# Kernel tuning notes

Measured on AMD Instinct MI355X. Metric: run time of the kernel, lower is better.

Reference implementation:

```python
import jax, jax.numpy as jnp
import numpy as np

D_MODEL, D_K, D_V, H = 512, 64, 64, 8
B, NQ, NK = 16, 784, 784
HW = 28  # sqrt(NQ)


def setup_inputs() -> dict:
    key = jax.random.key(0)
    ks = jax.random.split(key, 12)
    std = 0.001  # torch init.normal_(weight, std=0.001)
    return {
        "queries": jax.random.normal(ks[0], (B, NQ, D_MODEL), jnp.float32),
        "keys": jax.random.normal(ks[1], (B, NK, D_MODEL), jnp.float32),
        "values": jax.random.normal(ks[2], (B, NK, D_MODEL), jnp.float32),
        "self_corr": jax.random.normal(ks[3], (B, 1, NQ, NK), jnp.float32),
        # weights stored [in, out] for x @ W
        "Wq": jax.random.normal(ks[4], (D_MODEL, H * D_K), jnp.float32) * std,
        "bq": jnp.zeros((H * D_K,), jnp.float32),
        "Wk": jax.random.normal(ks[5], (D_MODEL, H * D_K), jnp.float32) * std,
        "bk": jnp.zeros((H * D_K,), jnp.float32),
        "Wv": jax.random.normal(ks[6], (D_MODEL, H * D_V), jnp.float32) * std,
        "bv": jnp.zeros((H * D_V,), jnp.float32),
        "Wo": jax.random.normal(ks[7], (H * D_V, D_MODEL), jnp.float32) * std,
        "bo": jnp.zeros((D_MODEL,), jnp.float32),
    }


def reference(queries, keys, values, self_corr, Wq, bq, Wk, bk, Wv, bv, Wo, bo):
    b, nq, cc = queries.shape
    nk = keys.shape[1]
    # projections -> [b, h, n, d]
    q = (queries @ Wq + bq).reshape(b, nq, H, D_K).transpose(0, 2, 1, 3)
    k = (keys @ Wk + bk).reshape(b, nk, H, D_K).transpose(0, 2, 1, 3)
    v = (values @ Wv + bv).reshape(b, nk, H, D_V).transpose(0, 2, 1, 3)
    # scaled scores [b, h, nq, nk]
    att_qk = jnp.einsum("bhqd,bhkd->bhqk", q, k) / np.sqrt(D_K).astype(np.float32)
    enhanced = att_qk + self_corr.reshape(b, -1, nq, nk)  # additive bias (broadcast over heads)
    attn = jax.nn.softmax(enhanced, axis=-1)
    # dropout is identity at inference (reference in eval mode)
    ctx = jnp.einsum("bhqk,bhkd->bhqd", attn, v)
    ctx = ctx.transpose(0, 2, 1, 3).reshape(b, nq, H * D_V)
    out = ctx @ Wo + bo  # [b, nq, d_model]
    hw = int(np.sqrt(nq))
    return out.transpose(0, 2, 1).reshape(b, cc, hw, hw)
```

## Files before the change

kernel.cpp:

```cpp
#include <hip/hip_runtime.h>

#define SZX ((size_t)12544 * 512)
#define WSEG ((size_t)262144)

typedef __attribute__((ext_vector_type(8))) short short8;
typedef __attribute__((ext_vector_type(4))) short short4s;
typedef __attribute__((ext_vector_type(4))) float floatx4;

typedef const __attribute__((address_space(1))) void* gas_cvp;
typedef __attribute__((address_space(3))) void* las_vp;

__device__ __forceinline__ void gl_lds16(const void* g, void* l) {
    __builtin_amdgcn_global_load_lds((gas_cvp)g, (las_vp)l, 16, 0, 0);
}

__device__ __forceinline__ unsigned short f2bf(float f) {
    unsigned int u = __float_as_uint(f);
    u += 0x7fffu + ((u >> 16) & 1u);
    return (unsigned short)(u >> 16);
}

__device__ __forceinline__ short8 lds_read8(const unsigned short* p) {
    short4s a = *(const short4s*)p;
    short4s b = *(const short4s*)(p + 4);
    return __builtin_shufflevector(a, b, 0, 1, 2, 3, 4, 5, 6, 7);
}

#define MFMA16(a, b, c) __builtin_amdgcn_mfma_f32_16x16x32_bf16(a, b, c, 0, 0, 0)

__global__ void cvt3(const float* __restrict__ q, const float* __restrict__ k,
                     const float* __restrict__ v,
                     unsigned short* __restrict__ xq, unsigned short* __restrict__ xk,
                     unsigned short* __restrict__ xv, int which) {
    int sel = blockIdx.y + which;
    const float* in = sel == 0 ? q : sel == 1 ? k : v;
    unsigned short* out = sel == 0 ? xq : sel == 1 ? xk : xv;
    size_t i = ((size_t)blockIdx.x * blockDim.x + threadIdx.x) * 4;
    float4 vv = *(const float4*)(in + i);
    ushort4 o = make_ushort4(f2bf(vv.x), f2bf(vv.y), f2bf(vv.z), f2bf(vv.w));
    *(ushort4*)(out + i) = o;
}

__global__ void transpose_cvt(const float* __restrict__ W0, const float* __restrict__ W1,
                              const float* __restrict__ W2, const float* __restrict__ W3,
                              unsigned short* __restrict__ out) {
    __shared__ float tile[32][33];
    const float* W = blockIdx.z == 0 ? W0 : blockIdx.z == 1 ? W1 : blockIdx.z == 2 ? W2 : W3;
    unsigned short* O = out + (size_t)blockIdx.z * WSEG;
    int x = blockIdx.x * 32 + threadIdx.x;
    int y0 = blockIdx.y * 32;
    for (int k = threadIdx.y; k < 32; k += 8)
        tile[k][threadIdx.x] = W[(size_t)(y0 + k) * 512 + x];
    __syncthreads();
    int xo = blockIdx.y * 32 + threadIdx.x;
    int yo0 = blockIdx.x * 32;
    for (int k = threadIdx.y; k < 32; k += 8)
        O[(size_t)(yo0 + k) * 512 + xo] = f2bf(tile[threadIdx.x][k]);
}

__global__ __launch_bounds__(256) void gemm_qkv(
    const unsigned short* __restrict__ Xq, const unsigned short* __restrict__ Xk,
    const unsigned short* __restrict__ Xv, const unsigned short* __restrict__ Wt,
    const float* __restrict__ bq, const float* __restrict__ bk, const float* __restrict__ bv,
    unsigned short* __restrict__ Qb, unsigned short* __restrict__ Kb,
    unsigned short* __restrict__ Vtb, int zoff)
{
    __shared__ unsigned short Als[128 * 32];
    __shared__ unsigned short Bls[128 * 32];
    int z = blockIdx.z + zoff;
    const unsigned short* X = z == 0 ? Xq : z == 1 ? Xk : Xv;
    const unsigned short* Wz = Wt + (size_t)z * WSEG;
    const float* bias = z == 0 ? bq : z == 1 ? bk : bv;

    int tid = threadIdx.x;
    int lane = tid & 63, wave = tid >> 6;
    int wm = wave & 1, wn = wave >> 1;
    int c16 = lane & 15, g = lane >> 4;
    int tm, tn;
    const unsigned short *Abase, *Bbase;
    if (z < 2) { tm = blockIdx.x; tn = blockIdx.y; Abase = X + (size_t)tm * 128 * 512; Bbase = Wz + (size_t)tn * 128 * 512; }
    else       { tm = blockIdx.y; tn = blockIdx.x; Abase = Wz + (size_t)tm * 128 * 512; Bbase = X + (size_t)tn * 128 * 512; }

    floatx4 acc[4][4];
#pragma unroll
    for (int i = 0; i < 4; i++)
#pragma unroll
        for (int j = 0; j < 4; j++) acc[i][j] = (floatx4){0.f, 0.f, 0.f, 0.f};

    for (int kb = 0; kb < 16; ++kb) {
        int k0 = kb * 32;
#pragma unroll
        for (int rep = 0; rep < 2; ++rep) {
            int slot = rep * 256 + tid;
            int row = slot >> 2, kp = slot & 3;
            gl_lds16(Abase + (size_t)row * 512 + k0 + kp * 8, &Als[slot * 8]);
            gl_lds16(Bbase + (size_t)row * 512 + k0 + kp * 8, &Bls[slot * 8]);
        }
        __syncthreads();
        short8 af[4], bfr[4];
#pragma unroll
        for (int i = 0; i < 4; i++)
            af[i] = *(const short8*)&Als[(wm * 64 + i * 16 + c16) * 32 + g * 8];
#pragma unroll
        for (int j = 0; j < 4; j++)
            bfr[j] = *(const short8*)&Bls[(wn * 64 + j * 16 + c16) * 32 + g * 8];
#pragma unroll
        for (int i = 0; i < 4; i++)
#pragma unroll
            for (int j = 0; j < 4; j++)
                acc[i][j] = MFMA16(af[i], bfr[j], acc[i][j]);
        __syncthreads();
    }

#pragma unroll
    for (int j = 0; j < 4; j++) {
        int n = tn * 128 + wn * 64 + j * 16 + c16;
        int bi = n / 784, nn = n - bi * 784;
        float bvn = (z < 2) ? bias[n] : 0.f;
#pragma unroll
        for (int i = 0; i < 4; i++) {
#pragma unroll
            for (int r4 = 0; r4 < 4; r4++) {
                int m = tm * 128 + wm * 64 + i * 16 + g * 4 + r4;
                float v = acc[i][j][r4] + ((z < 2) ? bvn : bias[m]);
                if (z == 0)      Qb[(size_t)m * 512 + n] = f2bf(v);
                else if (z == 1) Kb[(size_t)m * 512 + n] = f2bf(v);
                else {
                    int h = m >> 6, d = m & 63;
                    Vtb[(((size_t)bi * 8 + h) * 64 + d) * 784 + nn] = f2bf(v);
                }
            }
        }
    }
}

__global__ __launch_bounds__(256) void gemm_out(
    const unsigned short* __restrict__ Wto, const unsigned short* __restrict__ ctx,
    const float* __restrict__ bo, float* __restrict__ out)
{
    __shared__ unsigned short Als[64 * 32];
    __shared__ unsigned short Bls[128 * 32];
    int tid = threadIdx.x;
    int lane = tid & 63, wn = tid >> 6;
    int c16 = lane & 15, g = lane >> 4;
    int tm = blockIdx.x, tn = blockIdx.y;

    const unsigned short* Abase = Wto + (size_t)tm * 64 * 512;
    const unsigned short* Bbase = ctx + (size_t)tn * 128 * 512;

    floatx4 acc[4][2];
#pragma unroll
    for (int i = 0; i < 4; i++)
#pragma unroll
        for (int j = 0; j < 2; j++) acc[i][j] = (floatx4){0.f, 0.f, 0.f, 0.f};

    for (int kb = 0; kb < 16; ++kb) {
        int k0 = kb * 32;
        {
            int row = tid >> 2, kp = tid & 3;
            gl_lds16(Abase + (size_t)row * 512 + k0 + kp * 8, &Als[tid * 8]);
        }
#pragma unroll
        for (int rep = 0; rep < 2; ++rep) {
            int slot = rep * 256 + tid;
            int row = slot >> 2, kp = slot & 3;
            gl_lds16(Bbase + (size_t)row * 512 + k0 + kp * 8, &Bls[slot * 8]);
        }
        __syncthreads();
        short8 af[4], bfr[2];
#pragma unroll
        for (int i = 0; i < 4; i++)
            af[i] = *(const short8*)&Als[(i * 16 + c16) * 32 + g * 8];
#pragma unroll
        for (int j = 0; j < 2; j++)
            bfr[j] = *(const short8*)&Bls[(wn * 32 + j * 16 + c16) * 32 + g * 8];
#pragma unroll
        for (int i = 0; i < 4; i++)
#pragma unroll
            for (int j = 0; j < 2; j++)
                acc[i][j] = MFMA16(af[i], bfr[j], acc[i][j]);
        __syncthreads();
    }

#pragma unroll
    for (int j = 0; j < 2; j++) {
        int n = tn * 128 + wn * 32 + j * 16 + c16;
        int bi = n / 784, q = n - bi * 784;
#pragma unroll
        for (int i = 0; i < 4; i++) {
#pragma unroll
            for (int r4 = 0; r4 < 4; r4++) {
                int m = tm * 64 + i * 16 + g * 4 + r4;
                out[((size_t)bi * 512 + m) * 784 + q] = acc[i][j][r4] + bo[m];
            }
        }
    }
}

__global__ __launch_bounds__(256) void attn_kernel(
    const unsigned short* __restrict__ Qb,
    const unsigned short* __restrict__ Kb,
    const unsigned short* __restrict__ Vtb,
    const float* __restrict__ corr,
    unsigned short* __restrict__ ctx)
{
    __shared__ unsigned short Plds[2][4][2][16][68];
    int b = blockIdx.x, qt = blockIdx.y, hh = blockIdx.z;
    int tid = threadIdx.x;
    int lane = tid & 63, w = tid >> 6;
    int h = hh * 4 + w;
    int c16 = lane & 15, g = lane >> 4;
    int q0 = qt * 32;

    short8 aq[2][2];
#pragma unroll
    for (int u = 0; u < 2; ++u) {
        int row = q0 + u * 16 + c16; row = row < 784 ? row : 783;
        const unsigned short* qp = Qb + (size_t)(b * 784 + row) * 512 + h * 64 + g * 8;
        aq[u][0] = *(const short8*)qp;
        aq[u][1] = *(const short8*)(qp + 32);
    }

    floatx4 o[2][4];
    float l[2][4];
#pragma unroll
    for (int u = 0; u < 2; ++u)
#pragma unroll
        for (int nt = 0; nt < 4; nt++) { o[u][nt] = (floatx4){0.f, 0.f, 0.f, 0.f}; l[u][nt] = 0.f; }

    const float* corrb = corr + (size_t)b * 784 * 784;
    int crow[2][4];
#pragma unroll
    for (int u = 0; u < 2; ++u)
#pragma unroll
        for (int r = 0; r < 4; ++r) {
            int rr = q0 + u * 16 + g * 4 + r; rr = rr < 784 ? rr : 783;
            crow[u][r] = rr * 784;
        }

    const unsigned short* Vh = Vtb + ((size_t)(b * 8 + h)) * 64 * 784;
    const unsigned short* Kh = Kb + (size_t)b * 784 * 512 + h * 64;

    for (int it = 0; it < 13; ++it) {
        int k0 = it * 64;
        floatx4 s[2][4];
#pragma unroll
        for (int t = 0; t < 4; ++t) {
            int key = k0 + t * 16 + c16; key = key < 784 ? key : 783;
            const unsigned short* kp = Kh + (size_t)key * 512 + g * 8;
            short8 k0f = *(const short8*)kp;
            short8 k1f = *(const short8*)(kp + 32);
#pragma unroll
            for (int u = 0; u < 2; ++u) {
                floatx4 zz = (floatx4){0.f, 0.f, 0.f, 0.f};
                zz = MFMA16(aq[u][0], k0f, zz);
                zz = MFMA16(aq[u][1], k1f, zz);
                s[u][t] = zz;
            }
        }
        unsigned short* pbase = &Plds[it & 1][w][0][0][0];
#pragma unroll
        for (int u = 0; u < 2; ++u)
#pragma unroll
            for (int t = 0; t < 4; ++t) {
                int key = k0 + t * 16 + c16;
                bool valid = key < 784;
                int kc = valid ? key : 783;
#pragma unroll
                for (int r = 0; r < 4; ++r) {
                    float cv = corrb[crow[u][r] + kc];
                    float sv = fmaf(s[u][t][r], 0.125f, cv);
                    float pv = valid ? __expf(sv) : 0.f;
                    l[u][r] += pv;
                    pbase[(u * 16 + g * 4 + r) * 68 + t * 16 + c16] = f2bf(pv);
                }
            }
#pragma unroll
        for (int u = 0; u < 2; ++u) {
            const unsigned short* pr = &Plds[it & 1][w][u][c16][0];
            short8 pa0 = lds_read8(pr + g * 8);
            short8 pa1 = lds_read8(pr + 32 + g * 8);
#pragma unroll
            for (int nt = 0; nt < 4; ++nt) {
                int d = nt * 16 + c16;
                const unsigned short* vp = Vh + (size_t)d * 784 + k0 + g * 8;
                short8 v0 = *(const short8*)vp;
                short8 v1 = *(const short8*)(vp + 32);
                o[u][nt] = MFMA16(pa0, v0, o[u][nt]);
                o[u][nt] = MFMA16(pa1, v1, o[u][nt]);
            }
        }
    }

#pragma unroll
    for (int u = 0; u < 2; ++u)
#pragma unroll
        for (int r = 0; r < 4; ++r) {
            float lv = l[u][r];
            lv += __shfl_xor(lv, 1);
            lv += __shfl_xor(lv, 2);
            lv += __shfl_xor(lv, 4);
            lv += __shfl_xor(lv, 8);
            l[u][r] = 1.0f / lv;
        }
#pragma unroll
    for (int u = 0; u < 2; ++u)
#pragma unroll
        for (int r = 0; r < 4; ++r) {
            int row = q0 + u * 16 + g * 4 + r;
            if (row < 784) {
#pragma unroll
                for (int nt = 0; nt < 4; ++nt)
                    ctx[(size_t)(b * 784 + row) * 512 + h * 64 + nt * 16 + c16] =
                        f2bf(o[u][nt][r] * l[u][r]);
            }
        }
}

extern "C" void kernel_launch(void* const* d_in, const int* in_sizes, int n_in,
                              void* d_out, int out_size, void* d_ws, size_t ws_size,
                              hipStream_t stream) {
    (void)in_sizes; (void)n_in; (void)out_size;
    const float* queries = (const float*)d_in[0];
    const float* keys    = (const float*)d_in[1];
    const float* values  = (const float*)d_in[2];
    const float* corr    = (const float*)d_in[3];
    const float* Wq = (const float*)d_in[4];
    const float* bq = (const float*)d_in[5];
    const float* Wk = (const float*)d_in[6];
    const float* bk = (const float*)d_in[7];
    const float* Wv = (const float*)d_in[8];
    const float* bv = (const float*)d_in[9];
    const float* Wo = (const float*)d_in[10];
    const float* bo = (const float*)d_in[11];

    size_t need = (6 * SZX + 4 * WSEG) * 2;
    if (ws_size >= need) {
        unsigned short* Xq  = (unsigned short*)d_ws;
        unsigned short* Xk  = Xq + SZX;
        unsigned short* Xv  = Xk + SZX;
        unsigned short* Qb  = Xv + SZX;
        unsigned short* Kb  = Qb + SZX;
        unsigned short* Vtb = Kb + SZX;
        unsigned short* Wt  = Vtb + SZX;

        transpose_cvt<<<dim3(16, 16, 4), dim3(32, 8), 0, stream>>>(Wq, Wk, Wv, Wo, Wt);
        cvt3<<<dim3(6272, 3), 256, 0, stream>>>(queries, keys, values, Xq, Xk, Xv, 0);
        gemm_qkv<<<dim3(98, 4, 3), 256, 0, stream>>>(Xq, Xk, Xv, Wt, bq, bk, bv, Qb, Kb, Vtb, 0);
        attn_kernel<<<dim3(16, 25, 2), 256, 0, stream>>>(Qb, Kb, Vtb, corr, Xq);
        gemm_out<<<dim3(8, 98), 256, 0, stream>>>(Wt + 3 * WSEG, Xq, bo, (float*)d_out);
    } else {
        unsigned short* X   = (unsigned short*)d_ws;
        unsigned short* Qb  = X + SZX;
        unsigned short* Kb  = Qb + SZX;
        unsigned short* Vtb = Kb + SZX;
        unsigned short* Wt  = Vtb + SZX;

        transpose_cvt<<<dim3(16, 16, 4), dim3(32, 8), 0, stream>>>(Wq, Wk, Wv, Wo, Wt);
        for (int z = 0; z < 3; ++z) {
            cvt3<<<dim3(6272, 1), 256, 0, stream>>>(queries, keys, values, X, X, X, z);
            gemm_qkv<<<dim3(98, 4, 1), 256, 0, stream>>>(X, X, X, Wt, bq, bk, bv, Qb, Kb, Vtb, z);
        }
        attn_kernel<<<dim3(16, 25, 2), 256, 0, stream>>>(Qb, Kb, Vtb, corr, X);
        gemm_out<<<dim3(8, 98), 256, 0, stream>>>(Wt + 3 * WSEG, X, bo, (float*)d_out);
    }
}
```

Baseline: 326.4 us.

## Restructure attention to compute transposed scores with 16-query tiles and vector corr loads

```diff
diff --git a/kernel.cpp b/kernel.cpp
--- a/kernel.cpp
+++ b/kernel.cpp
@@ -1,4 +1,5 @@
 #include <hip/hip_runtime.h>
+#include <hip/hip_bf16.h>
 
 #define SZX ((size_t)12544 * 512)
 #define WSEG ((size_t)262144)
@@ -18,6 +19,11 @@
     unsigned int u = __float_as_uint(f);
     u += 0x7fffu + ((u >> 16) & 1u);
     return (unsigned short)(u >> 16);
+}
+
+__device__ __forceinline__ unsigned int pack2bf(float a, float b) {
+    __hip_bfloat162 h = __float22bfloat162_rn(float2{a, b});
+    return *(unsigned int*)&h;
 }
 
 __device__ __forceinline__ short8 lds_read8(const unsigned short* p) {
@@ -116,13 +122,12 @@
     for (int j = 0; j < 4; j++) {
         int n = tn * 128 + wn * 64 + j * 16 + c16;
         int bi = n / 784, nn = n - bi * 784;
-        float bvn = (z < 2) ? bias[n] : 0.f;
 #pragma unroll
         for (int i = 0; i < 4; i++) {
 #pragma unroll
             for (int r4 = 0; r4 < 4; r4++) {
                 int m = tm * 128 + wm * 64 + i * 16 + g * 4 + r4;
-                float v = acc[i][j][r4] + ((z < 2) ? bvn : bias[m]);
+                float v = acc[i][j][r4] + ((z < 2) ? bias[n] : bias[m]);
                 if (z == 0)      Qb[(size_t)m * 512 + n] = f2bf(v);
                 else if (z == 1) Kb[(size_t)m * 512 + n] = f2bf(v);
                 else {
@@ -197,123 +202,90 @@
     }
 }
 
-__global__ __launch_bounds__(256) void attn_kernel(
+__global__ __launch_bounds__(256, 4) void attn_kernel(
     const unsigned short* __restrict__ Qb,
     const unsigned short* __restrict__ Kb,
     const unsigned short* __restrict__ Vtb,
     const float* __restrict__ corr,
     unsigned short* __restrict__ ctx)
 {
-    __shared__ unsigned short Plds[2][4][2][16][68];
+    __shared__ unsigned short Plds[4][16][68];
     int b = blockIdx.x, qt = blockIdx.y, hh = blockIdx.z;
     int tid = threadIdx.x;
     int lane = tid & 63, w = tid >> 6;
     int h = hh * 4 + w;
     int c16 = lane & 15, g = lane >> 4;
-    int q0 = qt * 32;
-
-    short8 aq[2][2];
-#pragma unroll
-    for (int u = 0; u < 2; ++u) {
-        int row = q0 + u * 16 + c16; row = row < 784 ? row : 783;
-        const unsigned short* qp = Qb + (size_t)(b * 784 + row) * 512 + h * 64 + g * 8;
-        aq[u][0] = *(const short8*)qp;
-        aq[u][1] = *(const short8*)(qp + 32);
-    }
-
-    floatx4 o[2][4];
-    float l[2][4];
-#pragma unroll
-    for (int u = 0; u < 2; ++u)
-#pragma unroll
-        for (int nt = 0; nt < 4; nt++) { o[u][nt] = (floatx4){0.f, 0.f, 0.f, 0.f}; l[u][nt] = 0.f; }
-
-    const float* corrb = corr + (size_t)b * 784 * 784;
-    int crow[2][4];
-#pragma unroll
-    for (int u = 0; u < 2; ++u)
-#pragma unroll
-        for (int r = 0; r < 4; ++r) {
-            int rr = q0 + u * 16 + g * 4 + r; rr = rr < 784 ? rr : 783;
-            crow[u][r] = rr * 784;
-        }
-
+    int q0 = qt * 16;
+
+    short8 bq0, bq1;
+    {
+        const unsigned short* qp = Qb + (size_t)(b * 784 + q0 + c16) * 512 + h * 64 + g * 8;
+        bq0 = *(const short8*)qp;
+        bq1 = *(const short8*)(qp + 32);
+    }
+
+    floatx4 o[4];
+#pragma unroll
+    for (int nt = 0; nt < 4; nt++) o[nt] = (floatx4){0.f, 0.f, 0.f, 0.f};
+    float l = 0.f;
+
+    const float* corrq = corr + ((size_t)b * 784 + (q0 + c16)) * 784;
+    const unsigned short* Kh = Kb + (size_t)b * 784 * 512 + h * 64;
     const unsigned short* Vh = Vtb + ((size_t)(b * 8 + h)) * 64 * 784;
-    const unsigned short* Kh = Kb + (size_t)b * 784 * 512 + h * 64;
-
+
+#pragma unroll 1
     for (int it = 0; it < 13; ++it) {
         int k0 = it * 64;
-        floatx4 s[2][4];
 #pragma unroll
         for (int t = 0; t < 4; ++t) {
-            int key = k0 + t * 16 + c16; key = key < 784 ? key : 783;
-            const unsigned short* kp = Kh + (size_t)key * 512 + g * 8;
-            short8 k0f = *(const short8*)kp;
-            short8 k1f = *(const short8*)(kp + 32);
-#pragma unroll
-            for (int u = 0; u < 2; ++u) {
-                floatx4 zz = (floatx4){0.f, 0.f, 0.f, 0.f};
-                zz = MFMA16(aq[u][0], k0f, zz);
-                zz = MFMA16(aq[u][1], k1f, zz);
-                s[u][t] = zz;
+            int kbase = k0 + t * 16;
+            if (kbase < 784) {
+                const unsigned short* kp = Kh + (size_t)(kbase + c16) * 512 + g * 8;
+                short8 a0 = *(const short8*)kp;
+                short8 a1 = *(const short8*)(kp + 32);
+                floatx4 st = (floatx4){0.f, 0.f, 0.f, 0.f};
+                st = MFMA16(a0, bq0, st);
+                st = MFMA16(a1, bq1, st);
+                float4 cv = *(const float4*)(corrq + kbase + g * 4);
+                float e0 = __expf(fmaf(st[0], 0.125f, cv.x));
+                float e1 = __expf(fmaf(st[1], 0.125f, cv.y));
+                float e2 = __expf(fmaf(st[2], 0.125f, cv.z));
+                float e3 = __expf(fmaf(st[3], 0.125f, cv.w));
+                l += (e0 + e1) + (e2 + e3);
+                uint2 w2 = make_uint2(pack2bf(e0, e1), pack2bf(e2, e3));
+                *(uint2*)&Plds[w][c16][t * 16 + g * 4] = w2;
+            } else {
+                *(uint2*)&Plds[w][c16][t * 16 + g * 4] = make_uint2(0u, 0u);
             }
         }
-        unsigned short* pbase = &Plds[it & 1][w][0][0][0];
-#pragma unroll
-        for (int u = 0; u < 2; ++u)
-#pragma unroll
-            for (int t = 0; t < 4; ++t) {
-                int key = k0 + t * 16 + c16;
-                bool valid = key < 784;
-                int kc = valid ? key : 783;
-#pragma unroll
-                for (int r = 0; r < 4; ++r) {
-                    float cv = corrb[crow[u][r] + kc];
-                    float sv = fmaf(s[u][t][r], 0.125f, cv);
-                    float pv = valid ? __expf(sv) : 0.f;
-                    l[u][r] += pv;
-                    pbase[(u * 16 + g * 4 + r) * 68 + t * 16 + c16] = f2bf(pv);
-                }
-            }
-#pragma unroll
-        for (int u = 0; u < 2; ++u) {
-            const unsigned short* pr = &Plds[it & 1][w][u][c16][0];
-            short8 pa0 = lds_read8(pr + g * 8);
-            short8 pa1 = lds_read8(pr + 32 + g * 8);
-#pragma unroll
-            for (int nt = 0; nt < 4; ++nt) {
-                int d = nt * 16 + c16;
-                const unsigned short* vp = Vh + (size_t)d * 784 + k0 + g * 8;
-                short8 v0 = *(const short8*)vp;
-                short8 v1 = *(const short8*)(vp + 32);
-                o[u][nt] = MFMA16(pa0, v0, o[u][nt]);
-                o[u][nt] = MFMA16(pa1, v1, o[u][nt]);
-            }
-        }
-    }
-
-#pragma unroll
-    for (int u = 0; u < 2; ++u)
+        const unsigned short* prow = &Plds[w][c16][0];
+        short8 pa0 = lds_read8(prow + g * 8);
+        short8 pa1 = lds_read8(prow + 32 + g * 8);
+#pragma unroll
+        for (int nt = 0; nt < 4; ++nt) {
+            int d = nt * 16 + c16;
+            const unsigned short* vp = Vh + (size_t)d * 784 + k0 + g * 8;
+            short8 v0 = *(const short8*)vp;
+            short8 v1 = *(const short8*)(vp + 32);
+            o[nt] = MFMA16(pa0, v0, o[nt]);
+            o[nt] = MFMA16(pa1, v1, o[nt]);
+        }
+    }
+
+    l += __shfl_xor(l, 16);
+    l += __shfl_xor(l, 32);
+    float inv = 1.0f / l;
+    float invr[4];
+#pragma unroll
+    for (int r = 0; r < 4; ++r) invr[r] = __shfl(inv, g * 4 + r);
+
+#pragma unroll
+    for (int nt = 0; nt < 4; ++nt)
 #pragma unroll
         for (int r = 0; r < 4; ++r) {
-            float lv = l[u][r];
-            lv += __shfl_xor(lv, 1);
-            lv += __shfl_xor(lv, 2);
-            lv += __shfl_xor(lv, 4);
-            lv += __shfl_xor(lv, 8);
-            l[u][r] = 1.0f / lv;
-        }
-#pragma unroll
-    for (int u = 0; u < 2; ++u)
-#pragma unroll
-        for (int r = 0; r < 4; ++r) {
-            int row = q0 + u * 16 + g * 4 + r;
-            if (row < 784) {
-#pragma unroll
-                for (int nt = 0; nt < 4; ++nt)
-                    ctx[(size_t)(b * 784 + row) * 512 + h * 64 + nt * 16 + c16] =
-                        f2bf(o[u][nt][r] * l[u][r]);
-            }
+            int row = q0 + g * 4 + r;
+            ctx[(size_t)(b * 784 + row) * 512 + h * 64 + nt * 16 + c16] =
+                f2bf(o[nt][r] * invr[r]);
         }
 }
 
@@ -347,7 +319,7 @@
         transpose_cvt<<<dim3(16, 16, 4), dim3(32, 8), 0, stream>>>(Wq, Wk, Wv, Wo, Wt);
         cvt3<<<dim3(6272, 3), 256, 0, stream>>>(queries, keys, values, Xq, Xk, Xv, 0);
         gemm_qkv<<<dim3(98, 4, 3), 256, 0, stream>>>(Xq, Xk, Xv, Wt, bq, bk, bv, Qb, Kb, Vtb, 0);
-        attn_kernel<<<dim3(16, 25, 2), 256, 0, stream>>>(Qb, Kb, Vtb, corr, Xq);
+        attn_kernel<<<dim3(16, 49, 2), 256, 0, stream>>>(Qb, Kb, Vtb, corr, Xq);
         gemm_out<<<dim3(8, 98), 256, 0, stream>>>(Wt + 3 * WSEG, Xq, bo, (float*)d_out);
     } else {
         unsigned short* X   = (unsigned short*)d_ws;
@@ -361,7 +333,7 @@
             cvt3<<<dim3(6272, 1), 256, 0, stream>>>(queries, keys, values, X, X, X, z);
             gemm_qkv<<<dim3(98, 4, 1), 256, 0, stream>>>(X, X, X, Wt, bq, bk, bv, Qb, Kb, Vtb, z);
         }
-        attn_kernel<<<dim3(16, 25, 2), 256, 0, stream>>>(Qb, Kb, Vtb, corr, X);
+        attn_kernel<<<dim3(16, 49, 2), 256, 0, stream>>>(Qb, Kb, Vtb, corr, X);
         gemm_out<<<dim3(8, 98), 256, 0, stream>>>(Wt + 3 * WSEG, X, bo, (float*)d_out);
     }
 }
```

After: 395.6 us. 1.21x slower.
